# Kernel optimization log

Hardware: AMD Instinct MI355X
Metric: run time of the kernel (lower is better)

The kernel has to match this reference:

```python
import jax, jax.numpy as jnp
import numpy as np

B, S, D, H, DH = 4, 2048, 1024, 16, 64  # batch, seq, d_model, heads, head_dim


def setup_inputs() -> dict:
    key = jax.random.key(0)
    ks = jax.random.split(key, 5)
    sc_in = 1.0 / np.sqrt(D)
    return {
        "x": jax.random.normal(ks[0], (B, S, D), dtype=jnp.float32),
        "Wq": jax.random.normal(ks[1], (H, D, DH), dtype=jnp.float32) * sc_in,
        "Wk": jax.random.normal(ks[2], (H, D, DH), dtype=jnp.float32) * sc_in,
        "Wv": jax.random.normal(ks[3], (H, D, DH), dtype=jnp.float32) * sc_in,
        "Wo": jax.random.normal(ks[4], (D, D), dtype=jnp.float32) * sc_in,
        "bo": jnp.zeros((D,), dtype=jnp.float32),
    }


def reference(x, Wq, Wk, Wv, Wo, bo):
    # Per-head Q/K/V projections (all heads batched in one einsum each).
    q = jnp.einsum("bsd,hde->bhse", x, Wq)  # [B,H,S,DH]
    k = jnp.einsum("bsd,hde->bhse", x, Wk)
    v = jnp.einsum("bsd,hde->bhse", x, Wv)
    scale = 1.0 / jnp.sqrt(jnp.asarray(DH, dtype=x.dtype))
    scores = jnp.einsum("bhse,bhte->bhst", q, k) * scale  # [B,H,S,S]
    causal = jnp.tril(jnp.ones((S, S), dtype=bool))
    scores = jnp.where(causal, scores, jnp.asarray(-jnp.inf, dtype=scores.dtype))
    attn = jax.nn.softmax(scores, axis=-1)
    heads = jnp.einsum("bhst,bhte->bhse", attn, v)  # [B,H,S,DH]
    # Concat heads (head-major order matches torch.cat of per-head outputs).
    concat = heads.transpose(0, 2, 1, 3).reshape(B, S, D)
    out = jnp.einsum("bsd,df->bsf", concat, Wo) + bo
    return out  # dropout_rate = 0.0 -> identity
```

## Files before the change

### kernel.cpp

```cpp
#include <hip/hip_runtime.h>
#include <hip/hip_bf16.h>

typedef __attribute__((ext_vector_type(8))) short short8;
typedef __attribute__((ext_vector_type(4))) short short4x;
typedef __attribute__((ext_vector_type(4))) float floatx4;

__device__ __forceinline__ short f2bf(float f) {
    unsigned u = __float_as_uint(f);
    u = u + 0x7fffu + ((u >> 16) & 1u);
    return (short)(u >> 16);
}
__device__ __forceinline__ short f2bf_rz(float f) {
    return (short)(__float_as_uint(f) >> 16);
}

static constexpr int B_ = 4, S_ = 2048, D_ = 1024, H_ = 16, DH_ = 64;
static constexpr float QSCALE = 0.125f * 1.4426950408889634f;

__global__ __launch_bounds__(256) void convert_x(const float* __restrict__ in,
                                                 short* __restrict__ out, int n8) {
    int i = blockIdx.x * 256 + threadIdx.x;
    if (i >= n8) return;
    const float4* p = (const float4*)(in + (size_t)i * 8);
    float4 a = p[0], b = p[1];
    short8 v;
    v[0] = f2bf(a.x); v[1] = f2bf(a.y); v[2] = f2bf(a.z); v[3] = f2bf(a.w);
    v[4] = f2bf(b.x); v[5] = f2bf(b.y); v[6] = f2bf(b.z); v[7] = f2bf(b.w);
    *(short8*)(out + (size_t)i * 8) = v;
}

__global__ __launch_bounds__(256) void prep_weights(const float* __restrict__ Wq,
                                                    const float* __restrict__ Wk,
                                                    const float* __restrict__ Wv,
                                                    const float* __restrict__ Wo,
                                                    short* __restrict__ WqT,
                                                    short* __restrict__ WkT,
                                                    short* __restrict__ WvT,
                                                    short* __restrict__ WoT) {
    __shared__ alignas(16) float t[64 * 68];
    int z = blockIdx.z;
    const float* in;
    short* out;
    int N, M = D_, n0;
    if (z < 3) {
        const float* I = (z == 0) ? Wq : (z == 1) ? Wk : Wv;
        short* O = (z == 0) ? WqT : (z == 1) ? WkT : WvT;
        in = I + (size_t)blockIdx.y * D_ * DH_;
        out = O + (size_t)blockIdx.y * D_ * DH_;
        N = DH_; n0 = 0;
    } else {
        in = Wo; out = WoT; N = D_; n0 = blockIdx.y * 64;
    }
    int m0 = blockIdx.x * 64;
    int tid = threadIdx.x;
#pragma unroll
    for (int i = 0; i < 4; ++i) {
        int c = tid + i * 256;
        int row = c >> 4, c4 = (c & 15) * 4;
        float4 v = *(const float4*)(in + (size_t)(m0 + row) * N + n0 + c4);
        *(float4*)(t + row * 68 + c4) = v;
    }
    __syncthreads();
#pragma unroll
    for (int i = 0; i < 2; ++i) {
        int c = tid + i * 256;
        int row = c >> 3, c8 = (c & 7) * 8;
        short8 v;
#pragma unroll
        for (int j = 0; j < 8; ++j) v[j] = f2bf(t[(c8 + j) * 68 + row]);
        *(short8*)(out + (size_t)(n0 + row) * M + m0 + c8) = v;
    }
}

__device__ __forceinline__ void gemm128_core(const short* __restrict__ A,
                                             const short* __restrict__ Bm,
                                             short* ldsA, short* ldsB,
                                             int m0, int n0,
                                             floatx4 (&acc)[4][4],
                                             int w, int lane, int quad, int lm) {
    const int K = 1024;
    int wm = (w >> 1) * 64, wn = (w & 1) * 64;
    int rsub = lane >> 3;
    int csw = ((lane & 7) ^ rsub) * 8;
    int lmx = lm & 7;
    for (int k0 = 0; k0 < K; k0 += 64) {
#pragma unroll
        for (int i = 0; i < 4; ++i) {
            int r0 = w * 32 + i * 8;
            const short* ga = A + (size_t)(m0 + r0 + rsub) * K + k0 + csw;
            __builtin_amdgcn_global_load_lds((const __attribute__((address_space(1))) void*)ga,
                                             (__attribute__((address_space(3))) void*)(ldsA + r0 * 64),
                                             16, 0, 0);
            const short* gb = Bm + (size_t)(n0 + r0 + rsub) * K + k0 + csw;
            __builtin_amdgcn_global_load_lds((const __attribute__((address_space(1))) void*)gb,
                                             (__attribute__((address_space(3))) void*)(ldsB + r0 * 64),
                                             16, 0, 0);
        }
        __syncthreads();
#pragma unroll
        for (int ks = 0; ks < 2; ++ks) {
            short8 am[4], bn[4];
#pragma unroll
            for (int i = 0; i < 4; ++i)
                am[i] = *(const short8*)(ldsA + (wm + i * 16 + lm) * 64 + (((ks * 4 + quad) ^ lmx) << 3));
#pragma unroll
            for (int i = 0; i < 4; ++i)
                bn[i] = *(const short8*)(ldsB + (wn + i * 16 + lm) * 64 + (((ks * 4 + quad) ^ lmx) << 3));
#pragma unroll
            for (int mi = 0; mi < 4; ++mi)
#pragma unroll
                for (int ni = 0; ni < 4; ++ni)
                    acc[mi][ni] = __builtin_amdgcn_mfma_f32_16x16x32_bf16(am[mi], bn[ni], acc[mi][ni], 0, 0, 0);
        }
        __syncthreads();
    }
}

__global__ __launch_bounds__(256, 4) void qkv_gemm128(const short* __restrict__ xb,
                                                      const short* __restrict__ WqT,
                                                      const short* __restrict__ WkT,
                                                      const short* __restrict__ WvT,
                                                      short* __restrict__ Q,
                                                      short* __restrict__ K,
                                                      short* __restrict__ VT) {
    __shared__ alignas(16) short lds[16384];
    short* ldsA = lds;
    short* ldsB = lds + 8192;
    int m0 = blockIdx.x * 128, n0 = blockIdx.y * 128, z = blockIdx.z;
    const short* Bm = (z == 0) ? WqT : (z == 1) ? WkT : WvT;
    int tid = threadIdx.x, w = tid >> 6, lane = tid & 63, quad = lane >> 4, lm = lane & 15;

    floatx4 acc[4][4];
#pragma unroll
    for (int mi = 0; mi < 4; ++mi)
#pragma unroll
        for (int ni = 0; ni < 4; ++ni) acc[mi][ni] = (floatx4)0.0f;

    gemm128_core(xb, Bm, ldsA, ldsB, m0, n0, acc, w, lane, quad, lm);

    int wm = (w >> 1) * 64, wn = (w & 1) * 64;
    int b = m0 >> 11;
    int sbase = m0 & 2047;

    if (z < 2) {
        short* O = (z == 0) ? Q : K;
        float scale = (z == 0) ? QSCALE : 1.0f;
        short* t = lds;
#pragma unroll
        for (int ph = 0; ph < 2; ++ph) {
            if (ph) __syncthreads();
            if ((w & 1) == ph) {
#pragma unroll
                for (int mi = 0; mi < 4; ++mi)
#pragma unroll
                    for (int ni = 0; ni < 4; ++ni)
#pragma unroll
                        for (int r = 0; r < 4; ++r)
                            t[(wm + mi * 16 + quad * 4 + r) * 68 + ni * 16 + lm] =
                                f2bf(acc[mi][ni][r] * scale);
            }
            __syncthreads();
            int h = (n0 + ph * 64) >> 6;
            size_t obase = ((size_t)(b * 16 + h) * 2048 + sbase) * 64;
#pragma unroll
            for (int i = 0; i < 4; ++i) {
                int c = tid + i * 256;
                int m = c >> 3, e8 = (c & 7) * 8;
                short8 v = *(const short8*)(t + m * 68 + e8);
                *(short8*)(O + obase + (size_t)m * 64 + e8) = v;
            }
        }
    } else {
        short* t = lds;
#pragma unroll
        for (int ph = 0; ph < 2; ++ph) {
            if (ph) __syncthreads();
            if ((w & 1) == ph) {
#pragma unroll
                for (int mi = 0; mi < 4; ++mi)
#pragma unroll
                    for (int ni = 0; ni < 4; ++ni) {
                        int nl = ni * 16 + lm;
#pragma unroll
                        for (int r = 0; r < 4; ++r) {
                            int ml = wm + mi * 16 + quad * 4 + r;
                            t[nl * 136 + ml] = f2bf(acc[mi][ni][r]);
                        }
                    }
            }
            __syncthreads();
#pragma unroll
            for (int i = 0; i < 4; ++i) {
                int c = tid + i * 256;
                int rowl = c >> 4, colc = (c & 15) * 8;
                short8 v = *(const short8*)(t + rowl * 136 + colc);
                size_t n = n0 + ph * 64 + rowl;
                *(short8*)(VT + ((size_t)b * 1024 + n) * 2048 + sbase + colc) = v;
            }
        }
    }
}

__global__ __launch_bounds__(256, 4) void outproj128(const short* __restrict__ CC,
                                                     const short* __restrict__ WoT,
                                                     const float* __restrict__ bo,
                                                     float* __restrict__ out) {
    __shared__ alignas(16) short lds[16384];
    short* ldsA = lds;
    short* ldsB = lds + 8192;
    int m0 = blockIdx.x * 128, n0 = blockIdx.y * 128;
    int tid = threadIdx.x, w = tid >> 6, lane = tid & 63, quad = lane >> 4, lm = lane & 15;

    floatx4 acc[4][4];
#pragma unroll
    for (int mi = 0; mi < 4; ++mi)
#pragma unroll
        for (int ni = 0; ni < 4; ++ni) acc[mi][ni] = (floatx4)0.0f;

    gemm128_core(CC, WoT, ldsA, ldsB, m0, n0, acc, w, lane, quad, lm);

    int wm = (w >> 1) * 64, wn = (w & 1) * 64;
#pragma unroll
    for (int mi = 0; mi < 4; ++mi)
#pragma unroll
        for (int ni = 0; ni < 4; ++ni) {
            int n = n0 + wn + ni * 16 + lm;
            float bb = bo[n];
#pragma unroll
            for (int r = 0; r < 4; ++r) {
                int m = m0 + wm + mi * 16 + quad * 4 + r;
                out[(size_t)m * 1024 + n] = acc[mi][ni][r] + bb;
            }
        }
}

__global__ __launch_bounds__(256, 2) void attn_kernel(const short* __restrict__ Q,
                                                      const short* __restrict__ Kb,
                                                      const short* __restrict__ VT,
                                                      short* __restrict__ CC) {
    __shared__ alignas(16) short Kt[128 * 64];
    __shared__ alignas(16) short Vt[64 * 128];
    __shared__ alignas(16) short Pt[128 * 128];
    int bh = blockIdx.x;
    int pi = blockIdx.y;
    int b = bh >> 4, h = bh & 15;
    int tid = threadIdx.x;
    int w = tid >> 6, l = tid & 63;
    int quad = l >> 4, lm = l & 15;
    int lmx = lm & 7;
    int rsub = l >> 3;
    int csw = ((l & 7) ^ rsub) * 8;
    int vr4 = l >> 4;
    int vc = l & 15;

    const short* Qbh = Q + (size_t)bh * S_ * DH_;
    const short* Kbh = Kb + (size_t)bh * S_ * DH_;
    const short* Vbh = VT + (size_t)bh * 64 * S_;

    for (int ps = 0; ps < 2; ++ps) {
        int qt = ps ? (15 - pi) : pi;
        int q0 = qt * 128;

        short8 qa[2][2];
#pragma unroll
        for (int nq = 0; nq < 2; ++nq) {
            const short* Qrow = Qbh + (size_t)(q0 + nq * 64 + w * 16 + lm) * DH_;
            qa[nq][0] = *(const short8*)(Qrow + quad * 8);
            qa[nq][1] = *(const short8*)(Qrow + 32 + quad * 8);
        }

        floatx4 acc_o[2][4];
#pragma unroll
        for (int nq = 0; nq < 2; ++nq)
#pragma unroll
            for (int ct = 0; ct < 4; ++ct) acc_o[nq][ct] = (floatx4)0.0f;
        float lsum[2] = {0.0f, 0.0f};

        int nkt = qt + 1;
        for (int kt = 0; kt < nkt; ++kt) {
            int t0 = kt * 128;
            const short* Ktile = Kbh + (size_t)t0 * DH_;
#pragma unroll
            for (int i = 0; i < 4; ++i) {
                int r0 = w * 32 + i * 8;
                const short* ga = Ktile + (size_t)(r0 + rsub) * 64 + csw;
                __builtin_amdgcn_global_load_lds((const __attribute__((address_space(1))) void*)ga,
                                                 (__attribute__((address_space(3))) void*)(Kt + r0 * 64),
                                                 16, 0, 0);
            }
#pragma unroll
            for (int i = 0; i < 4; ++i) {
                int r0v = w * 16 + i * 4;
                int row = r0v + vr4;
                const short* gv = Vbh + (size_t)row * S_ + t0 + ((vc ^ (row & 7)) * 8);
                __builtin_amdgcn_global_load_lds((const __attribute__((address_space(1))) void*)gv,
                                                 (__attribute__((address_space(3))) void*)(Vt + r0v * 128),
                                                 16, 0, 0);
            }
            __syncthreads();

            short8 kf[8][2];
#pragma unroll
            for (int mt = 0; mt < 8; ++mt)
#pragma unroll
                for (int ks = 0; ks < 2; ++ks)
                    kf[mt][ks] = *(const short8*)(Kt + (mt * 16 + lm) * 64 + (((ks * 4 + quad) ^ lmx) << 3));

            bool last = (kt == nkt - 1);
#pragma unroll
            for (int nq = 0; nq < 2; ++nq) {
                floatx4 sc[8];
                __builtin_amdgcn_s_setprio(1);
#pragma unroll
                for (int mt = 0; mt < 8; ++mt) {
                    floatx4 t = (floatx4)0.0f;
                    t = __builtin_amdgcn_mfma_f32_16x16x32_bf16(kf[mt][0], qa[nq][0], t, 0, 0, 0);
                    t = __builtin_amdgcn_mfma_f32_16x16x32_bf16(kf[mt][1], qa[nq][1], t, 0, 0, 0);
                    sc[mt] = t;
                }
                __builtin_amdgcn_s_setprio(0);
                if (last) {
                    int q_ = q0 + nq * 64 + w * 16 + lm;
#pragma unroll
                    for (int mt = 0; mt < 8; ++mt)
#pragma unroll
                        for (int r = 0; r < 4; ++r) {
                            int t_ = t0 + mt * 16 + quad * 4 + r;
                            if (t_ > q_) sc[mt][r] = -INFINITY;
                        }
                }
                int prow = nq * 64 + w * 16 + lm;
#pragma unroll
                for (int mt = 0; mt < 8; ++mt) {
                    float p0 = exp2f(sc[mt][0]);
                    float p1 = exp2f(sc[mt][1]);
                    float p2 = exp2f(sc[mt][2]);
                    float p3 = exp2f(sc[mt][3]);
                    lsum[nq] += (p0 + p1) + (p2 + p3);
                    short4x pk;
                    pk[0] = f2bf_rz(p0); pk[1] = f2bf_rz(p1);
                    pk[2] = f2bf_rz(p2); pk[3] = f2bf_rz(p3);
                    int c = mt * 2 + (quad >> 1);
                    *(short4x*)(Pt + prow * 128 + ((c ^ lmx) << 3) + (quad & 1) * 4) = pk;
                }
            }
            short8 pa[2][4];
#pragma unroll
            for (int nq = 0; nq < 2; ++nq)
#pragma unroll
                for (int ks = 0; ks < 4; ++ks)
                    pa[nq][ks] = *(const short8*)(Pt + (nq * 64 + w * 16 + lm) * 128 +
                                                  (((ks * 4 + quad) ^ lmx) << 3));
            __builtin_amdgcn_s_setprio(1);
#pragma unroll
            for (int ct = 0; ct < 4; ++ct) {
                const short* vrow = Vt + (ct * 16 + lm) * 128;
#pragma unroll
                for (int ks = 0; ks < 4; ++ks) {
                    short8 v = *(const short8*)(vrow + (((ks * 4 + quad) ^ lmx) << 3));
                    acc_o[0][ct] = __builtin_amdgcn_mfma_f32_16x16x32_bf16(pa[0][ks], v, acc_o[0][ct], 0, 0, 0);
                    acc_o[1][ct] = __builtin_amdgcn_mfma_f32_16x16x32_bf16(pa[1][ks], v, acc_o[1][ct], 0, 0, 0);
                }
            }
            __builtin_amdgcn_s_setprio(0);
            __syncthreads();
        }

        float invl[2];
#pragma unroll
        for (int nq = 0; nq < 2; ++nq) {
            float lr = lsum[nq];
            lr += __shfl_xor(lr, 16);
            lr += __shfl_xor(lr, 32);
            invl[nq] = 1.0f / lr;
        }

#pragma unroll
        for (int nq = 0; nq < 2; ++nq) {
#pragma unroll
            for (int r = 0; r < 4; ++r) {
                float iv = __shfl(invl[nq], quad * 4 + r);
                int row = q0 + nq * 64 + w * 16 + quad * 4 + r;
                short* OC = CC + ((size_t)b * S_ + row) * D_ + h * DH_;
#pragma unroll
                for (int ct = 0; ct < 4; ++ct)
                    OC[ct * 16 + lm] = f2bf(acc_o[nq][ct][r] * iv);
            }
        }
    }
}

extern "C" void kernel_launch(void* const* d_in, const int* in_sizes, int n_in,
                              void* d_out, int out_size, void* d_ws, size_t ws_size,
                              hipStream_t stream) {
    const float* x  = (const float*)d_in[0];
    const float* Wq = (const float*)d_in[1];
    const float* Wk = (const float*)d_in[2];
    const float* Wv = (const float*)d_in[3];
    const float* Wo = (const float*)d_in[4];
    const float* bo = (const float*)d_in[5];
    float* out = (float*)d_out;
    short* ws = (short*)d_ws;

    const size_t WSZ = (size_t)H_ * D_ * DH_;
    const size_t QSZ = (size_t)B_ * H_ * S_ * DH_;
    short* WqT = ws;
    short* WkT = WqT + WSZ;
    short* WvT = WkT + WSZ;
    short* WoT = WvT + WSZ;
    short* xb  = WoT + (size_t)D_ * D_;
    short* Qb  = xb + (size_t)B_ * S_ * D_;
    short* Kb  = Qb + QSZ;
    short* VTb = Kb + QSZ;
    short* CCb = VTb + QSZ;

    convert_x<<<(B_ * S_ * D_ / 8 + 255) / 256, 256, 0, stream>>>(x, xb, B_ * S_ * D_ / 8);
    prep_weights<<<dim3(16, 16, 4), 256, 0, stream>>>(Wq, Wk, Wv, Wo, WqT, WkT, WvT, WoT);
    qkv_gemm128<<<dim3(64, 8, 3), 256, 0, stream>>>(xb, WqT, WkT, WvT, Qb, Kb, VTb);
    attn_kernel<<<dim3(64, 8), 256, 0, stream>>>(Qb, Kb, VTb, CCb);
    outproj128<<<dim3(64, 8), 256, 0, stream>>>(CCb, WoT, bo, out);
}
```

Before: 247.0 us.

## Prefetch next K/V tile into registers during attention compute

```diff
diff --git a/kernel.cpp b/kernel.cpp
--- a/kernel.cpp
+++ b/kernel.cpp
@@ -277,27 +277,45 @@
         float lsum[2] = {0.0f, 0.0f};
 
         int nkt = qt + 1;
+
+        __syncthreads();
+#pragma unroll
+        for (int i = 0; i < 4; ++i) {
+            int r0 = w * 32 + i * 8;
+            const short* ga = Kbh + (size_t)(r0 + rsub) * 64 + csw;
+            __builtin_amdgcn_global_load_lds((const __attribute__((address_space(1))) void*)ga,
+                                             (__attribute__((address_space(3))) void*)(Kt + r0 * 64),
+                                             16, 0, 0);
+        }
+#pragma unroll
+        for (int i = 0; i < 4; ++i) {
+            int r0v = w * 16 + i * 4;
+            int row = r0v + vr4;
+            const short* gv = Vbh + (size_t)row * S_ + ((vc ^ (row & 7)) * 8);
+            __builtin_amdgcn_global_load_lds((const __attribute__((address_space(1))) void*)gv,
+                                             (__attribute__((address_space(3))) void*)(Vt + r0v * 128),
+                                             16, 0, 0);
+        }
+        __syncthreads();
+
         for (int kt = 0; kt < nkt; ++kt) {
             int t0 = kt * 128;
-            const short* Ktile = Kbh + (size_t)t0 * DH_;
-#pragma unroll
-            for (int i = 0; i < 4; ++i) {
-                int r0 = w * 32 + i * 8;
-                const short* ga = Ktile + (size_t)(r0 + rsub) * 64 + csw;
-                __builtin_amdgcn_global_load_lds((const __attribute__((address_space(1))) void*)ga,
-                                                 (__attribute__((address_space(3))) void*)(Kt + r0 * 64),
-                                                 16, 0, 0);
-            }
-#pragma unroll
-            for (int i = 0; i < 4; ++i) {
-                int r0v = w * 16 + i * 4;
-                int row = r0v + vr4;
-                const short* gv = Vbh + (size_t)row * S_ + t0 + ((vc ^ (row & 7)) * 8);
-                __builtin_amdgcn_global_load_lds((const __attribute__((address_space(1))) void*)gv,
-                                                 (__attribute__((address_space(3))) void*)(Vt + r0v * 128),
-                                                 16, 0, 0);
-            }
-            __syncthreads();
+            bool pf = (kt + 1 < nkt);
+            short8 kpre[4], vpre[4];
+            if (pf) {
+                int t1 = t0 + 128;
+                const short* Ktile = Kbh + (size_t)t1 * DH_;
+#pragma unroll
+                for (int i = 0; i < 4; ++i) {
+                    int r0 = w * 32 + i * 8;
+                    kpre[i] = *(const short8*)(Ktile + (size_t)(r0 + rsub) * 64 + csw);
+                }
+#pragma unroll
+                for (int i = 0; i < 4; ++i) {
+                    int row = w * 16 + i * 4 + vr4;
+                    vpre[i] = *(const short8*)(Vbh + (size_t)row * S_ + t1 + ((vc ^ (row & 7)) * 8));
+                }
+            }
 
             short8 kf[8][2];
 #pragma unroll
@@ -363,7 +381,21 @@
                 }
             }
             __builtin_amdgcn_s_setprio(0);
-            __syncthreads();
+
+            if (pf) {
+                __syncthreads();
+#pragma unroll
+                for (int i = 0; i < 4; ++i) {
+                    int r0 = w * 32 + i * 8;
+                    *(short8*)(Kt + r0 * 64 + l * 8) = kpre[i];
+                }
+#pragma unroll
+                for (int i = 0; i < 4; ++i) {
+                    int r0v = w * 16 + i * 4;
+                    *(short8*)(Vt + r0v * 128 + l * 8) = vpre[i];
+                }
+                __syncthreads();
+            }
         }
 
         float invl[2];
```

Measured after the change: 250.8 us. No clear change (+1.5%).
